# Optimization experiments

Measured on AMD Instinct MI355X. Metric: run time of the kernel, lower is better.

## Reference

```python
import math
import jax, jax.numpy as jnp
import numpy as np

B, S, D_MODEL, N_HEADS, D_KV = 8, 1024, 1024, 16, 64
INNER = N_HEADS * D_KV
NUM_BUCKETS, MAX_DISTANCE = 32, 128


def _relative_position_bucket(relative_position, bidirectional=True,
                              num_buckets=NUM_BUCKETS, max_distance=MAX_DISTANCE):
    # Faithful port of T5Attention._relative_position_bucket (int math).
    relative_buckets = jnp.zeros_like(relative_position)
    if bidirectional:
        num_buckets //= 2
        relative_buckets += (relative_position > 0).astype(jnp.int32) * num_buckets
        relative_position = jnp.abs(relative_position)
    else:
        relative_position = -jnp.minimum(relative_position, 0)
    max_exact = num_buckets // 2
    is_small = relative_position < max_exact
    # clamp to >=1 before log to avoid -inf -> int cast (value unused when is_small)
    rp_f = jnp.maximum(relative_position, 1).astype(jnp.float32)
    rel_if_large = max_exact + (
        jnp.log(rp_f / max_exact) / math.log(max_distance / max_exact)
        * (num_buckets - max_exact)
    ).astype(jnp.int32)
    rel_if_large = jnp.minimum(rel_if_large, num_buckets - 1)
    relative_buckets += jnp.where(is_small, relative_position, rel_if_large)
    return relative_buckets


def compute_bias(rel_bias_emb, query_length, key_length):
    context_position = jnp.arange(query_length, dtype=jnp.int32)[:, None]
    memory_position = jnp.arange(key_length, dtype=jnp.int32)[None, :]
    relative_position = memory_position - context_position  # [Q, K]
    buckets = _relative_position_bucket(relative_position, bidirectional=True)
    values = rel_bias_emb[buckets]                 # [Q, K, H]
    return jnp.transpose(values, (2, 0, 1))[None]  # [1, H, Q, K]


def setup_inputs() -> dict:
    key = jax.random.key(0)
    k1, k2, k3, k4 = jax.random.split(key, 4)
    return {
        "hidden_states": jax.random.normal(k1, (B, S, D_MODEL), jnp.float32),
        "w_qkv": jax.random.normal(k2, (3 * INNER, D_MODEL), jnp.float32) * 0.02,
        "rel_bias_emb": jax.random.normal(k3, (NUM_BUCKETS, N_HEADS), jnp.float32) * 0.02,
        "w_out": jax.random.normal(k4, (D_MODEL, INNER), jnp.float32) * 0.02,
    }


def reference(hidden_states, w_qkv, rel_bias_emb, w_out):
    # QKV projection (no bias)
    qkv = jnp.einsum('bsd,ed->bse', hidden_states, w_qkv)  # [B,S,3*INNER]
    q, k, v = jnp.split(qkv, 3, axis=-1)
    q = q.reshape(B, S, N_HEADS, D_KV)
    k = k.reshape(B, S, N_HEADS, D_KV)
    v = v.reshape(B, S, N_HEADS, D_KV)
    # T5 attention uses scale = 1.0 (no 1/sqrt(d))
    scores = jnp.einsum('bqhd,bkhd->bhqk', q, k)           # [B,H,S,S]
    scores = scores + compute_bias(rel_bias_emb, S, S)     # additive rel-pos bias
    probs = jax.nn.softmax(scores, axis=-1)
    attn = jnp.einsum('bhqk,bkhd->bqhd', probs, v).reshape(B, S, INNER)
    return jnp.einsum('bsi,di->bsd', attn, w_out)          # out_proj, no bias
```

## Files before the change

kernel.cpp:

```cpp
#include <hip/hip_runtime.h>
#include <math.h>

typedef __attribute__((ext_vector_type(8))) short short8;
typedef __attribute__((ext_vector_type(4))) float f32x4;
typedef __attribute__((ext_vector_type(16))) float f32x16;
typedef __attribute__((ext_vector_type(4))) int int32x4;
typedef unsigned short bf16_t;

#define GLOAD_LDS16(g, l)                                                   \
    __builtin_amdgcn_global_load_lds(                                       \
        (__attribute__((address_space(1))) void*)(g),                       \
        (__attribute__((address_space(3))) void*)(l), 16, 0, 0)

__device__ __forceinline__ bf16_t f2b_rne(float f) {
    unsigned int u = __float_as_uint(f);
    u += 0x7FFFu + ((u >> 16) & 1u);
    return (bf16_t)(u >> 16);
}

__global__ __launch_bounds__(256) void f2b_kernel(const float* __restrict__ in,
                                                  bf16_t* __restrict__ out, int n4) {
    int stride = gridDim.x * 256;
    for (int i = blockIdx.x * 256 + threadIdx.x; i < n4; i += stride) {
        float4 v = ((const float4*)in)[i];
        ushort4 p;
        p.x = f2b_rne(v.x); p.y = f2b_rne(v.y);
        p.z = f2b_rne(v.z); p.w = f2b_rne(v.w);
        ((ushort4*)out)[i] = p;
    }
}

__global__ void build_bias_tab(const float* __restrict__ emb, float* __restrict__ tab) {
    int idx = blockIdx.x * 256 + threadIdx.x;
    if (idx >= 2047) return;
    int rel = idx - 1023;
    int rb = rel > 0 ? 16 : 0;
    int rp = rel < 0 ? -rel : rel;
    int bucket;
    if (rp < 8) {
        bucket = rb + rp;
    } else {
        float t = logf((float)rp * 0.125f);
        int vi = 8 + (int)(t / 2.772588722239781f * 8.0f);
        bucket = rb + (vi < 15 ? vi : 15);
    }
    #pragma unroll
    for (int hh = 0; hh < 16; hh++)
        tab[hh * 2048 + idx] = emb[bucket * 16 + hh];
}

template <int MODE, typename OT>
__global__ __launch_bounds__(256) void gemm_mfma(const bf16_t* __restrict__ A,
                                                 const bf16_t* __restrict__ B,
                                                 OT* __restrict__ C, int N, int gx,
                                                 bf16_t* __restrict__ qlin,
                                                 bf16_t* __restrict__ klin,
                                                 bf16_t* __restrict__ vlin) {
    __shared__ __align__(16) bf16_t As[128 * 32];
    __shared__ __align__(16) bf16_t Bs[128 * 32];
    const int nwg = gridDim.x;
    const int cpx = nwg >> 3;
    const int swz = (blockIdx.x & 7) * cpx + (blockIdx.x >> 3);
    const int bx = swz % gx, by = swz / gx;

    const int tid = threadIdx.x;
    const int lane = tid & 63;
    const int wv = tid >> 6;
    const int wr = wv >> 1, wc = wv & 1;
    const int m0 = by * 128, n0 = bx * 128;
    const int cc = lane & 15, cg = lane >> 4;

    f32x4 acc[4][4];
    #pragma unroll
    for (int i = 0; i < 4; i++)
        #pragma unroll
        for (int j = 0; j < 4; j++) acc[i][j] = {0.f, 0.f, 0.f, 0.f};

    const int rsw = (cc >> 1) & 3;

    for (int k0 = 0; k0 < 1024; k0 += 32) {
        __syncthreads();
        #pragma unroll
        for (int it = 0; it < 2; it++) {
            int c = it * 256 + tid;
            int r = c >> 2, sl = c & 3;
            int kc = (sl ^ ((r >> 1) & 3)) * 8;
            GLOAD_LDS16(A + (size_t)(m0 + r) * 1024 + k0 + kc, &As[c * 8]);
            GLOAD_LDS16(B + (size_t)(n0 + r) * 1024 + k0 + kc, &Bs[c * 8]);
        }
        __syncthreads();

        short8 af[4], bf[4];
        #pragma unroll
        for (int mf = 0; mf < 4; mf++)
            af[mf] = *(const short8*)&As[(wr * 64 + mf * 16 + cc) * 32 + (cg ^ rsw) * 8];
        #pragma unroll
        for (int nf = 0; nf < 4; nf++)
            bf[nf] = *(const short8*)&Bs[(wc * 64 + nf * 16 + cc) * 32 + (cg ^ rsw) * 8];
        #pragma unroll
        for (int mf = 0; mf < 4; mf++)
            #pragma unroll
            for (int nf = 0; nf < 4; nf++)
                acc[mf][nf] = __builtin_amdgcn_mfma_f32_16x16x32_bf16(
                    af[mf], bf[nf], acc[mf][nf], 0, 0, 0);
    }

    if constexpr (MODE == 0) {
        #pragma unroll
        for (int mf = 0; mf < 4; mf++)
            #pragma unroll
            for (int j = 0; j < 4; j++) {
                size_t row = (size_t)(m0 + wr * 64 + mf * 16 + cg * 4 + j);
                OT* cp = C + row * N + n0 + wc * 64 + cc;
                #pragma unroll
                for (int nf = 0; nf < 4; nf++) cp[nf * 16] = acc[mf][nf][j];
            }
    } else {
        __shared__ bf16_t Es[64 * 136];
        const int part = n0 >> 10;
        const int hbase = (n0 & 1023) >> 6;
        const int bI = m0 >> 10;
        const int seq0 = m0 & 1023;

        for (int half = 0; half < 2; half++) {
            __syncthreads();
            if (wr == half) {
                #pragma unroll
                for (int mf = 0; mf < 4; mf++)
                    #pragma unroll
                    for (int j = 0; j < 4; j++) {
                        int rl = mf * 16 + cg * 4 + j;
                        #pragma unroll
                        for (int nf = 0; nf < 4; nf++)
                            Es[rl * 136 + wc * 64 + nf * 16 + cc] = f2b_rne(acc[mf][nf][j]);
                    }
            }
            __syncthreads();
            const int th = (seq0 + half * 64) >> 5;
            #pragma unroll
            for (int it = 0; it < 4; it++) {
                int g = it * 256 + tid;
                int hh = g >> 9, t2 = (g >> 8) & 1, ii = (g >> 6) & 3, l16 = g & 63;
                size_t bh = (size_t)(bI * 16 + hbase + hh);
                if (part == 2) {
                    int d = (ii >> 1) * 32 + (l16 & 31);
                    int sb = t2 * 32 + (ii & 1) * 16 + (l16 >> 5) * 8;
                    short8 v;
                    #pragma unroll
                    for (int j = 0; j < 8; j++)
                        v[j] = (short)Es[(sb + j) * 136 + hh * 64 + d];
                    *(short8*)(vlin + (((bh * 32 + th + t2) * 4 + ii) * 64 + l16) * 8) = v;
                } else {
                    int row = t2 * 32 + (l16 & 31);
                    int d0 = ii * 16 + (l16 >> 5) * 8;
                    short8 v = *(const short8*)&Es[row * 136 + hh * 64 + d0];
                    bf16_t* dst = (part == 0) ? qlin : klin;
                    *(short8*)(dst + (((bh * 32 + th + t2) * 4 + ii) * 64 + l16) * 8) = v;
                }
            }
        }
    }
}

__global__ __launch_bounds__(256, 3) void attn_mfma4(const bf16_t* __restrict__ qlin,
                                                     const float* __restrict__ tab,
                                                     const bf16_t* __restrict__ klin,
                                                     const bf16_t* __restrict__ vlin,
                                                     bf16_t* __restrict__ attn_out) {
    __shared__ float bias2[2304];
    __shared__ bf16_t Ol[4 * 32 * 68];

    const int i = blockIdx.x;
    const int g = ((i >> 6) << 3) + (i & 7);
    const int qc = (i >> 3) & 7;
    const int b = g >> 4, h = g & 15;
    const int q0 = qc * 128;

    const int tid = threadIdx.x;
    const int lane = tid & 63;
    const int w = tid >> 6;
    const int l31 = lane & 31;
    const int hi = lane >> 5;

    const float* tabh = tab + h * 2048;
    const int wbase = 896 - q0;
    #pragma unroll
    for (int it = 0; it < 5; it++) {
        int j = it * 256 + tid;
        if (j < 1151) {
            bias2[2 * j]     = tabh[wbase + j];
            bias2[2 * j + 1] = tabh[wbase + j + 1];
        }
    }

    const bf16_t* ql = qlin + (size_t)g * 65536;
    const bf16_t* kl = klin + (size_t)g * 65536;
    const bf16_t* vl = vlin + (size_t)g * 65536;

    const int qloc = w * 32 + l31;
    const int qt = qc * 4 + w;
    short8 qf[4];
    #pragma unroll
    for (int s = 0; s < 4; s++)
        qf[s] = *(const short8*)(ql + (size_t)qt * 2048 + s * 512 + lane * 8);

    f32x16 O0 = (f32x16)0.f, O1 = (f32x16)0.f;
    float m_run = -1e30f, l_run = 0.f;

    auto loadk = [&](short8 (&dst)[4], int kt) {
        const bf16_t* kp = kl + (size_t)kt * 2048 + lane * 8;
        #pragma unroll
        for (int s = 0; s < 4; s++) dst[s] = *(const short8*)(kp + s * 512);
    };

    auto compute = [&](short8 (&kf)[4], int kt) {
        const int k0 = kt * 32;
        const bf16_t* vp = vl + (size_t)kt * 2048 + lane * 8;
        short8 vf0 = *(const short8*)vp;
        short8 vf1 = *(const short8*)(vp + 512);
        short8 vf2 = *(const short8*)(vp + 1024);
        short8 vf3 = *(const short8*)(vp + 1536);

        f32x16 S = (f32x16)0.f;
        #pragma unroll
        for (int s = 0; s < 4; s++)
            S = __builtin_amdgcn_mfma_f32_32x32x16_bf16(kf[s], qf[s], S, 0, 0, 0);

        float p[16];
        #pragma unroll
        for (int gg = 0; gg < 4; gg++) {
            int bi = k0 + 8 * gg + 4 * hi + 127 - qloc;
            float2 b0 = *(const float2*)&bias2[2 * bi];
            float2 b1 = *(const float2*)&bias2[2 * (bi + 2)];
            p[4 * gg + 0] = S[4 * gg + 0] + b0.x;
            p[4 * gg + 1] = S[4 * gg + 1] + b0.y;
            p[4 * gg + 2] = S[4 * gg + 2] + b1.x;
            p[4 * gg + 3] = S[4 * gg + 3] + b1.y;
        }

        float pmax = p[0];
        #pragma unroll
        for (int r = 1; r < 16; r++) pmax = fmaxf(pmax, p[r]);
        pmax = fmaxf(pmax, __shfl_xor(pmax, 32));
        if (!__all(pmax - m_run <= 8.f)) {
            float mn = fmaxf(m_run, pmax);
            float sc = __expf(m_run - mn);
            l_run *= sc;
            #pragma unroll
            for (int r = 0; r < 16; r++) { O0[r] *= sc; O1[r] *= sc; }
            m_run = mn;
        }
        float rsum = 0.f;
        #pragma unroll
        for (int r = 0; r < 16; r++) { p[r] = __expf(p[r] - m_run); rsum += p[r]; }
        rsum += __shfl_xor(rsum, 32);
        l_run += rsum;

        unsigned int wv[8];
        #pragma unroll
        for (int ii = 0; ii < 8; ii++) {
            unsigned int t;
            asm("v_cvt_pk_bf16_f32 %0, %1, %2" : "=v"(t) : "v"(p[2 * ii]), "v"(p[2 * ii + 1]));
            wv[ii] = t;
        }
        unsigned int x0 = __shfl_xor(hi ? wv[0] : wv[2], 32);
        unsigned int x1 = __shfl_xor(hi ? wv[1] : wv[3], 32);
        unsigned int x2 = __shfl_xor(hi ? wv[4] : wv[6], 32);
        unsigned int x3 = __shfl_xor(hi ? wv[5] : wv[7], 32);
        int32x4 pf0i, pf1i;
        if (hi) {
            pf0i = (int32x4){(int)x0, (int)x1, (int)wv[2], (int)wv[3]};
            pf1i = (int32x4){(int)x2, (int)x3, (int)wv[6], (int)wv[7]};
        } else {
            pf0i = (int32x4){(int)wv[0], (int)wv[1], (int)x0, (int)x1};
            pf1i = (int32x4){(int)wv[4], (int)wv[5], (int)x2, (int)x3};
        }
        short8 pf0 = __builtin_bit_cast(short8, pf0i);
        short8 pf1 = __builtin_bit_cast(short8, pf1i);

        O0 = __builtin_amdgcn_mfma_f32_32x32x16_bf16(vf0, pf0, O0, 0, 0, 0);
        O0 = __builtin_amdgcn_mfma_f32_32x32x16_bf16(vf1, pf1, O0, 0, 0, 0);
        O1 = __builtin_amdgcn_mfma_f32_32x32x16_bf16(vf2, pf0, O1, 0, 0, 0);
        O1 = __builtin_amdgcn_mfma_f32_32x32x16_bf16(vf3, pf1, O1, 0, 0, 0);
    };

    __syncthreads();

    short8 kA[4], kB[4];
    loadk(kA, 0);
    for (int kt = 0; kt < 32; kt += 2) {
        loadk(kB, kt + 1);
        compute(kA, kt);
        if (kt < 30) loadk(kA, kt + 2);
        compute(kB, kt + 1);
    }

    float inv = 1.f / l_run;
    bf16_t* olw = &Ol[w * 32 * 68];
    #pragma unroll
    for (int r = 0; r < 16; r++) {
        int dr = (r & 3) + 8 * (r >> 2) + 4 * hi;
        olw[l31 * 68 + dr]      = f2b_rne(O0[r] * inv);
        olw[l31 * 68 + dr + 32] = f2b_rne(O1[r] * inv);
    }
    bf16_t* outp = attn_out + (size_t)(b * 1024 + q0 + w * 32) * 1024 + h * 64;
    #pragma unroll 4
    for (int i2 = 0; i2 < 32; i2++)
        outp[(size_t)i2 * 1024 + lane] = olw[i2 * 68 + lane];
}

extern "C" void kernel_launch(void* const* d_in, const int* in_sizes, int n_in,
                              void* d_out, int out_size, void* d_ws, size_t ws_size,
                              hipStream_t stream) {
    const float* hs   = (const float*)d_in[0];
    const float* wqkv = (const float*)d_in[1];
    const float* emb  = (const float*)d_in[2];
    const float* wout = (const float*)d_in[3];
    float* out = (float*)d_out;

    char* p = (char*)d_ws;
    bf16_t* hsb   = (bf16_t*)p; p += (size_t)8192 * 1024 * 2;
    bf16_t* wqkvb = (bf16_t*)p; p += (size_t)3072 * 1024 * 2;
    bf16_t* woutb = (bf16_t*)p; p += (size_t)1024 * 1024 * 2;
    bf16_t* qlin  = (bf16_t*)p; p += (size_t)128 * 65536 * 2;
    bf16_t* klin  = (bf16_t*)p; p += (size_t)128 * 65536 * 2;
    bf16_t* vlin  = (bf16_t*)p; p += (size_t)128 * 65536 * 2;
    bf16_t* attnb = (bf16_t*)p; p += (size_t)8192 * 1024 * 2;
    float*  tab   = (float*)p;

    f2b_kernel<<<2048, 256, 0, stream>>>(hs, hsb, 8192 * 1024 / 4);
    f2b_kernel<<<768, 256, 0, stream>>>(wqkv, wqkvb, 3072 * 1024 / 4);
    f2b_kernel<<<256, 256, 0, stream>>>(wout, woutb, 1024 * 1024 / 4);
    build_bias_tab<<<8, 256, 0, stream>>>(emb, tab);

    gemm_mfma<1, bf16_t><<<1536, 256, 0, stream>>>(hsb, wqkvb, (bf16_t*)nullptr, 3072, 24,
                                                   qlin, klin, vlin);
    attn_mfma4<<<1024, 256, 0, stream>>>(qlin, tab, klin, vlin, attnb);
    gemm_mfma<0, float><<<512, 256, 0, stream>>>(attnb, woutb, out, 1024, 8,
                                                 nullptr, nullptr, nullptr);
}
```

Before: 249.1 us.

## Double GEMM K-tile, fold log2e into bias and use exp2 with max3 reductions

The GEMM k-step grows from 32 to 64 with a wider XOR swizzle, halving barriers and loop iterations per output tile. LDS is merged into one shared buffer reused for the epilogue staging. In attention, log2(e) is folded into the bias table and the score FMA, so softmax uses raw v_exp_f32 (exp2), and the max and sum reductions use v_max3 and tree adds. The larger tile doubles LDS per block, which may reduce occupancy. The 8.0 rescale threshold now sits in the log2 domain.

```diff
diff --git a/kernel.cpp b/kernel.cpp
--- a/kernel.cpp
+++ b/kernel.cpp
@@ -7,6 +7,8 @@
 typedef __attribute__((ext_vector_type(4))) int int32x4;
 typedef unsigned short bf16_t;
 
+#define L2E 1.44269504089f
+
 #define GLOAD_LDS16(g, l)                                                   \
     __builtin_amdgcn_global_load_lds(                                       \
         (__attribute__((address_space(1))) void*)(g),                       \
@@ -16,6 +18,18 @@
     unsigned int u = __float_as_uint(f);
     u += 0x7FFFu + ((u >> 16) & 1u);
     return (bf16_t)(u >> 16);
+}
+
+__device__ __forceinline__ float max3f(float a, float b, float c) {
+    float d;
+    asm("v_max3_f32 %0, %1, %2, %3" : "=v"(d) : "v"(a), "v"(b), "v"(c));
+    return d;
+}
+
+__device__ __forceinline__ float exp2_fast(float x) {
+    float r;
+    asm("v_exp_f32 %0, %1" : "=v"(r) : "v"(x));
+    return r;
 }
 
 __global__ __launch_bounds__(256) void f2b_kernel(const float* __restrict__ in,
@@ -46,7 +60,7 @@
     }
     #pragma unroll
     for (int hh = 0; hh < 16; hh++)
-        tab[hh * 2048 + idx] = emb[bucket * 16 + hh];
+        tab[hh * 2048 + idx] = emb[bucket * 16 + hh] * L2E;
 }
 
 template <int MODE, typename OT>
@@ -56,8 +70,10 @@
                                                  bf16_t* __restrict__ qlin,
                                                  bf16_t* __restrict__ klin,
                                                  bf16_t* __restrict__ vlin) {
-    __shared__ __align__(16) bf16_t As[128 * 32];
-    __shared__ __align__(16) bf16_t Bs[128 * 32];
+    __shared__ __align__(16) char smem[32768];
+    bf16_t* As = (bf16_t*)smem;
+    bf16_t* Bs = (bf16_t*)(smem + 16384);
+
     const int nwg = gridDim.x;
     const int cpx = nwg >> 3;
     const int swz = (blockIdx.x & 7) * cpx + (blockIdx.x >> 3);
@@ -76,33 +92,38 @@
         #pragma unroll
         for (int j = 0; j < 4; j++) acc[i][j] = {0.f, 0.f, 0.f, 0.f};
 
-    const int rsw = (cc >> 1) & 3;
-
-    for (int k0 = 0; k0 < 1024; k0 += 32) {
+    const int rsw = cc & 7;
+
+    for (int k0 = 0; k0 < 1024; k0 += 64) {
         __syncthreads();
         #pragma unroll
-        for (int it = 0; it < 2; it++) {
+        for (int it = 0; it < 4; it++) {
             int c = it * 256 + tid;
-            int r = c >> 2, sl = c & 3;
-            int kc = (sl ^ ((r >> 1) & 3)) * 8;
+            int r = c >> 3, sl = c & 7;
+            int kc = (sl ^ (r & 7)) * 8;
             GLOAD_LDS16(A + (size_t)(m0 + r) * 1024 + k0 + kc, &As[c * 8]);
             GLOAD_LDS16(B + (size_t)(n0 + r) * 1024 + k0 + kc, &Bs[c * 8]);
         }
         __syncthreads();
 
-        short8 af[4], bf[4];
-        #pragma unroll
-        for (int mf = 0; mf < 4; mf++)
-            af[mf] = *(const short8*)&As[(wr * 64 + mf * 16 + cc) * 32 + (cg ^ rsw) * 8];
-        #pragma unroll
-        for (int nf = 0; nf < 4; nf++)
-            bf[nf] = *(const short8*)&Bs[(wc * 64 + nf * 16 + cc) * 32 + (cg ^ rsw) * 8];
-        #pragma unroll
-        for (int mf = 0; mf < 4; mf++)
+        #pragma unroll
+        for (int h = 0; h < 2; h++) {
+            short8 af[4], bf[4];
+            #pragma unroll
+            for (int mf = 0; mf < 4; mf++)
+                af[mf] = *(const short8*)&As[(wr * 64 + mf * 16 + cc) * 64 +
+                                             ((h * 4 + cg) ^ rsw) * 8];
             #pragma unroll
             for (int nf = 0; nf < 4; nf++)
-                acc[mf][nf] = __builtin_amdgcn_mfma_f32_16x16x32_bf16(
-                    af[mf], bf[nf], acc[mf][nf], 0, 0, 0);
+                bf[nf] = *(const short8*)&Bs[(wc * 64 + nf * 16 + cc) * 64 +
+                                             ((h * 4 + cg) ^ rsw) * 8];
+            #pragma unroll
+            for (int mf = 0; mf < 4; mf++)
+                #pragma unroll
+                for (int nf = 0; nf < 4; nf++)
+                    acc[mf][nf] = __builtin_amdgcn_mfma_f32_16x16x32_bf16(
+                        af[mf], bf[nf], acc[mf][nf], 0, 0, 0);
+        }
     }
 
     if constexpr (MODE == 0) {
@@ -116,7 +137,7 @@
                 for (int nf = 0; nf < 4; nf++) cp[nf * 16] = acc[mf][nf][j];
             }
     } else {
-        __shared__ bf16_t Es[64 * 136];
+        bf16_t* Es = (bf16_t*)smem;
         const int part = n0 >> 10;
         const int hbase = (n0 & 1023) >> 6;
         const int bI = m0 >> 10;
@@ -132,7 +153,8 @@
                         int rl = mf * 16 + cg * 4 + j;
                         #pragma unroll
                         for (int nf = 0; nf < 4; nf++)
-                            Es[rl * 136 + wc * 64 + nf * 16 + cc] = f2b_rne(acc[mf][nf][j]);
+                            Es[rl * 136 + wc * 64 + nf * 16 + cc] =
+                                f2b_rne(acc[mf][nf][j]);
                     }
             }
             __syncthreads();
@@ -232,48 +254,56 @@
             int bi = k0 + 8 * gg + 4 * hi + 127 - qloc;
             float2 b0 = *(const float2*)&bias2[2 * bi];
             float2 b1 = *(const float2*)&bias2[2 * (bi + 2)];
-            p[4 * gg + 0] = S[4 * gg + 0] + b0.x;
-            p[4 * gg + 1] = S[4 * gg + 1] + b0.y;
-            p[4 * gg + 2] = S[4 * gg + 2] + b1.x;
-            p[4 * gg + 3] = S[4 * gg + 3] + b1.y;
-        }
-
-        float pmax = p[0];
-        #pragma unroll
-        for (int r = 1; r < 16; r++) pmax = fmaxf(pmax, p[r]);
+            p[4 * gg + 0] = fmaf(S[4 * gg + 0], L2E, b0.x);
+            p[4 * gg + 1] = fmaf(S[4 * gg + 1], L2E, b0.y);
+            p[4 * gg + 2] = fmaf(S[4 * gg + 2], L2E, b1.x);
+            p[4 * gg + 3] = fmaf(S[4 * gg + 3], L2E, b1.y);
+        }
+
+        float t0 = max3f(p[0], p[1], p[2]);
+        float t1 = max3f(p[3], p[4], p[5]);
+        float t2 = max3f(p[6], p[7], p[8]);
+        float t3 = max3f(p[9], p[10], p[11]);
+        float t4 = max3f(p[12], p[13], p[14]);
+        float u0 = max3f(t0, t1, p[15]);
+        float pmax = fmaxf(u0, max3f(t2, t3, t4));
         pmax = fmaxf(pmax, __shfl_xor(pmax, 32));
         if (!__all(pmax - m_run <= 8.f)) {
             float mn = fmaxf(m_run, pmax);
-            float sc = __expf(m_run - mn);
+            float sc = exp2_fast(m_run - mn);
             l_run *= sc;
             #pragma unroll
             for (int r = 0; r < 16; r++) { O0[r] *= sc; O1[r] *= sc; }
             m_run = mn;
         }
-        float rsum = 0.f;
-        #pragma unroll
-        for (int r = 0; r < 16; r++) { p[r] = __expf(p[r] - m_run); rsum += p[r]; }
+        #pragma unroll
+        for (int r = 0; r < 16; r++) p[r] = exp2_fast(p[r] - m_run);
+        float s0 = (p[0] + p[1]) + (p[2] + p[3]);
+        float s1 = (p[4] + p[5]) + (p[6] + p[7]);
+        float s2 = (p[8] + p[9]) + (p[10] + p[11]);
+        float s3 = (p[12] + p[13]) + (p[14] + p[15]);
+        float rsum = (s0 + s1) + (s2 + s3);
         rsum += __shfl_xor(rsum, 32);
         l_run += rsum;
 
-        unsigned int wv[8];
+        unsigned int wvv[8];
         #pragma unroll
         for (int ii = 0; ii < 8; ii++) {
             unsigned int t;
             asm("v_cvt_pk_bf16_f32 %0, %1, %2" : "=v"(t) : "v"(p[2 * ii]), "v"(p[2 * ii + 1]));
-            wv[ii] = t;
-        }
-        unsigned int x0 = __shfl_xor(hi ? wv[0] : wv[2], 32);
-        unsigned int x1 = __shfl_xor(hi ? wv[1] : wv[3], 32);
-        unsigned int x2 = __shfl_xor(hi ? wv[4] : wv[6], 32);
-        unsigned int x3 = __shfl_xor(hi ? wv[5] : wv[7], 32);
+            wvv[ii] = t;
+        }
+        unsigned int x0 = __shfl_xor(hi ? wvv[0] : wvv[2], 32);
+        unsigned int x1 = __shfl_xor(hi ? wvv[1] : wvv[3], 32);
+        unsigned int x2 = __shfl_xor(hi ? wvv[4] : wvv[6], 32);
+        unsigned int x3 = __shfl_xor(hi ? wvv[5] : wvv[7], 32);
         int32x4 pf0i, pf1i;
         if (hi) {
-            pf0i = (int32x4){(int)x0, (int)x1, (int)wv[2], (int)wv[3]};
-            pf1i = (int32x4){(int)x2, (int)x3, (int)wv[6], (int)wv[7]};
+            pf0i = (int32x4){(int)x0, (int)x1, (int)wvv[2], (int)wvv[3]};
+            pf1i = (int32x4){(int)x2, (int)x3, (int)wvv[6], (int)wvv[7]};
         } else {
-            pf0i = (int32x4){(int)wv[0], (int)wv[1], (int)x0, (int)x1};
-            pf1i = (int32x4){(int)wv[4], (int)wv[5], (int)x2, (int)x3};
+            pf0i = (int32x4){(int)wvv[0], (int)wvv[1], (int)x0, (int)x1};
+            pf1i = (int32x4){(int)wvv[4], (int)wvv[5], (int)x2, (int)x3};
         }
         short8 pf0 = __builtin_bit_cast(short8, pf0i);
         short8 pf1 = __builtin_bit_cast(short8, pf1i);
```

Measured after the change: 246.7 us. Within noise of the previous version (-1.0%).
